# Optimization experiments

Measured on AMD Instinct MI355X. Metric: run time of the kernel, lower is better.

## Reference

```python
import jax, jax.numpy as jnp
import numpy as np

EMBED_DIM = 256; NUM_HEADS = 8; NUM_LEVELS = 4; NUM_POINTS = 4; FFN_DIM = 1024
SHAPES = [(128, 128), (64, 64), (32, 32), (16, 16)]
LN_EPS = 1e-5


def setup_inputs() -> dict:
    key = jax.random.key(0)
    ks = jax.random.split(key, 12)
    B = 2; C = EMBED_DIM
    Lin = sum(h * w for h, w in SHAPES)
    starts = np.concatenate([[0], np.cumsum([h * w for h, w in SHAPES])[:-1]])
    MLP2 = NUM_HEADS * NUM_LEVELS * NUM_POINTS
    p = lambda k, *s: jax.random.normal(k, s, jnp.float32) * 0.05
    return {
        "src": jax.random.normal(ks[0], (B, Lin, C), jnp.float32),
        "pos": jax.random.normal(ks[1], (B, Lin, C), jnp.float32),
        "reference_points": jax.random.uniform(ks[2], (B, Lin, NUM_LEVELS, 2), jnp.float32),
        "Wv": p(ks[3], C, C), "bv": jnp.zeros((C,), jnp.float32),
        "Wo": p(ks[4], C, MLP2 * 2),
        "bo": jax.random.uniform(ks[5], (MLP2 * 2,), jnp.float32, -2.0, 2.0),
        "Wa": p(ks[6], C, MLP2), "ba": jnp.zeros((MLP2,), jnp.float32),
        "Wout": p(ks[7], C, C), "bout": jnp.zeros((C,), jnp.float32),
        "gamma": jnp.ones((C,), jnp.float32), "beta": jnp.zeros((C,), jnp.float32),
        "W1": p(ks[8], C, FFN_DIM), "b1": jnp.zeros((FFN_DIM,), jnp.float32),
        "W2": p(ks[9], FFN_DIM, C), "b2": jnp.zeros((C,), jnp.float32),
        "spatial_shapes": jnp.array(SHAPES, dtype=jnp.int32),
        "level_start_index": jnp.array(starts, dtype=jnp.int32),
        "padding_mask": jnp.zeros((B, Lin), dtype=bool),
    }


def _layer_norm(x, g, b):
    m = jnp.mean(x, axis=-1, keepdims=True)
    v = jnp.mean((x - m) ** 2, axis=-1, keepdims=True)
    return (x - m) * jax.lax.rsqrt(v + LN_EPS) * g + b


def _bilinear_sample(val, loc, H, W):
    # val: [B, M, H*W, D]; loc: [B, M, Q, P, 2] normalized [0,1] (x, y)
    # matches torch grid_sample(align_corners=False, padding_mode='zeros')
    x = loc[..., 0] * W - 0.5
    y = loc[..., 1] * H - 0.5
    x0 = jnp.floor(x); y0 = jnp.floor(y)
    lx = x - x0; ly = y - y0
    x0 = x0.astype(jnp.int32); y0 = y0.astype(jnp.int32)
    Bm, M, Q, P = x0.shape
    out = jnp.zeros(val.shape[:2] + (Q, P, val.shape[-1]), val.dtype)
    corners = ((0, 0, (1 - lx) * (1 - ly)), (1, 0, lx * (1 - ly)),
               (0, 1, (1 - lx) * ly), (1, 1, lx * ly))
    for dx, dy, w in corners:
        xi = x0 + dx; yi = y0 + dy
        valid = (xi >= 0) & (xi < W) & (yi >= 0) & (yi < H)
        idx = jnp.clip(yi, 0, H - 1) * W + jnp.clip(xi, 0, W - 1)  # [B,M,Q,P]
        g = jnp.take_along_axis(val, idx.reshape(Bm, M, Q * P, 1), axis=2)
        g = g.reshape(Bm, M, Q, P, -1)
        out = out + (w * valid)[..., None] * g
    return out  # [B, M, Q, P, D]


def _forward(src, pos, reference_points, Wv, bv, Wo, bo, Wa, ba, Wout, bout,
             gamma, beta, W1, b1, W2, b2, spatial_shapes, level_start_index,
             padding_mask):
    M, L, P = NUM_HEADS, NUM_LEVELS, NUM_POINTS
    B, Lin, C = src.shape
    D = C // M
    shapes = np.asarray(spatial_shapes)          # static level geometry
    starts = np.asarray(level_start_index)
    query = src + pos
    value = src @ Wv + bv
    value = jnp.where(padding_mask[..., None], 0.0, value)
    value = value.reshape(B, Lin, M, D).transpose(0, 2, 1, 3)  # [B,M,Lin,D]
    Lq = query.shape[1]
    off = (query @ Wo + bo).reshape(B, Lq, M, L, P, 2)
    attn = jax.nn.softmax((query @ Wa + ba).reshape(B, Lq, M, L * P), axis=-1)
    attn = attn.reshape(B, Lq, M, L, P).transpose(0, 2, 1, 3, 4)  # [B,M,Lq,L,P]
    # offset normalizer is (W, H) per level
    normalizer = jnp.stack([spatial_shapes[:, 1], spatial_shapes[:, 0]], -1).astype(src.dtype)
    loc = reference_points[:, :, None, :, None, :] + off / normalizer[None, None, None, :, None, :]
    loc = loc.transpose(0, 2, 1, 3, 4, 5)  # [B,M,Lq,L,P,2]
    out = jnp.zeros((B, Lq, M, D), src.dtype)
    for l in range(L):
        H, W = int(shapes[l, 0]), int(shapes[l, 1])
        s = int(starts[l])
        vl = value[:, :, s:s + H * W, :]
        samp = _bilinear_sample(vl, loc[:, :, :, l], H, W)  # [B,M,Lq,P,D]
        out = out + jnp.einsum('bmqp,bmqpd->bqmd', attn[:, :, :, l], samp)
    src2 = out.reshape(B, Lq, C) @ Wout + bout
    x = _layer_norm(src + src2, gamma, beta)   # residual + norm (dropout is eval identity)
    h = jax.nn.relu(x @ W1 + b1)               # Mlp, no second residual in this module
    return h @ W2 + b2


def reference(src, pos, reference_points, Wv, bv, Wo, bo, Wa, ba, Wout, bout,
              gamma, beta, W1, b1, W2, b2, spatial_shapes, level_start_index,
              padding_mask):
    return _forward(src, pos, reference_points, Wv, bv, Wo, bo, Wa, ba, Wout,
                    bout, gamma, beta, W1, b1, W2, b2, spatial_shapes,
                    level_start_index, padding_mask)
```

## Files before the change

kernel.cpp:

```cpp
#include <hip/hip_runtime.h>
#include <hip/hip_bf16.h>
#include <math.h>

#define B_SZ   2
#define LIN    21760
#define C_DIM  256
#define M_H    8
#define D_H    32
#define NLEV   4
#define NPTS   4
#define FFN    1024
#define NTOK   (B_SZ * LIN)
#define LN_EPS 1e-5f

typedef __bf16 bf16;
typedef bf16  bf16x4 __attribute__((ext_vector_type(4)));
typedef bf16  bf16x8 __attribute__((ext_vector_type(8)));
typedef float f32x4  __attribute__((ext_vector_type(4)));

__device__ __constant__ int c_Ht[4] = {128, 64, 32, 16};
__device__ __constant__ int c_Wt[4] = {128, 64, 32, 16};
__device__ __constant__ int c_St[4] = {0, 16384, 20480, 21504};

static __device__ __forceinline__ float bf2f(unsigned short u) {
    union { float f; unsigned int i; } c;
    c.i = ((unsigned int)u) << 16;
    return c.f;
}

__global__ __launch_bounds__(256) void k_conv(const float* __restrict__ src,
                                              const float* __restrict__ pos,
                                              bf16* __restrict__ srcb,
                                              bf16* __restrict__ qb) {
    const int i = blockIdx.x * 256 + threadIdx.x;
    const float4 s4 = ((const float4*)src)[i];
    const float4 p4 = ((const float4*)pos)[i];
    bf16x4 sb, qb4;
    sb.x = (bf16)s4.x; sb.y = (bf16)s4.y; sb.z = (bf16)s4.z; sb.w = (bf16)s4.w;
    qb4.x = (bf16)(s4.x + p4.x); qb4.y = (bf16)(s4.y + p4.y);
    qb4.z = (bf16)(s4.z + p4.z); qb4.w = (bf16)(s4.w + p4.w);
    ((bf16x4*)srcb)[i] = sb;
    ((bf16x4*)qb)[i]   = qb4;
}

__global__ __launch_bounds__(256) void k_wt(const float* __restrict__ W,
                                            bf16* __restrict__ Wt,
                                            int K, int N, int nTilesN) {
    __shared__ float tile[32][33];
    const int bx = blockIdx.x % nTilesN;
    const int by = blockIdx.x / nTilesN;
    const int tx = threadIdx.x & 31, ty = threadIdx.x >> 5;
    const int n0 = bx * 32, k0 = by * 32;
#pragma unroll
    for (int i = 0; i < 32; i += 8)
        tile[ty + i][tx] = W[(long)(k0 + ty + i) * N + n0 + tx];
    __syncthreads();
#pragma unroll
    for (int i = 0; i < 32; i += 8)
        Wt[(long)(n0 + ty + i) * K + k0 + tx] = (bf16)tile[tx][ty + i];
}

#define GEMM_PROLOG(Aptr)                                                     \
    const int t = threadIdx.x;                                                \
    const int lane = t & 63, w = t >> 6;                                      \
    const int c0 = lane & 15, kg = lane >> 4;                                 \
    const long tok0 = (long)blockIdx.x * 32;                                  \
    {                                                                         \
        const bf16x8* src8 = (const bf16x8*)((Aptr) + tok0 * C_DIM);          \
        bf16x8* dst8 = (bf16x8*)xs;                                           \
        for (int i = t; i < 1024; i += 256)                                   \
            dst8[i ^ ((i >> 5) & 7)] = src8[i];                               \
    }                                                                         \
    __syncthreads();                                                          \
    bf16x8 afr[2][8];                                                         \
    _Pragma("unroll")                                                         \
    for (int mh = 0; mh < 2; ++mh) {                                          \
        const int m = mh * 16 + c0;                                           \
        _Pragma("unroll")                                                     \
        for (int kc = 0; kc < 8; ++kc) {                                      \
            const int chunk = m * 32 + kc * 4 + kg;                           \
            afr[mh][kc] = ((const bf16x8*)xs)[chunk ^ (m & 7)];               \
        }                                                                     \
    }

__global__ __launch_bounds__(256) void k_value_mfma(const bf16* __restrict__ A,
                                                    const bf16* __restrict__ Bw,
                                                    const float* __restrict__ bv,
                                                    bf16* __restrict__ value) {
    __shared__ bf16 xs[32 * 256];
    GEMM_PROLOG(A)

    const int b = (int)(tok0 / LIN);
    const int qbase = (int)(tok0 - (long)b * LIN);

#pragma unroll
    for (int nt = 0; nt < 4; ++nt) {
        const int n = w * 64 + nt * 16 + c0;
        f32x4 a0 = {0.f, 0.f, 0.f, 0.f};
        f32x4 a1 = {0.f, 0.f, 0.f, 0.f};
        const bf16* wrow = Bw + (long)n * 256 + kg * 8;
#pragma unroll
        for (int kc = 0; kc < 8; ++kc) {
            const bf16x8 bfr = *(const bf16x8*)(wrow + kc * 32);
            a0 = __builtin_amdgcn_mfma_f32_16x16x32_bf16(afr[0][kc], bfr, a0, 0, 0, 0);
            a1 = __builtin_amdgcn_mfma_f32_16x16x32_bf16(afr[1][kc], bfr, a1, 0, 0, 0);
        }
        const float bb = bv[n];
        const int m = n >> 5, d = n & 31;
        bf16* vb = value + ((long)(b * M_H + m) * LIN) * D_H + d;
#pragma unroll
        for (int r = 0; r < 4; ++r) {
            const int q0 = qbase + kg * 4 + r;
            vb[(long)q0 * D_H]        = (bf16)(a0[r] + bb);
            vb[(long)(q0 + 16) * D_H] = (bf16)(a1[r] + bb);
        }
    }
}

__global__ __launch_bounds__(256) void k_qloc_mfma(const bf16* __restrict__ A,
                                                   const bf16* __restrict__ Bw,
                                                   const float* __restrict__ bo,
                                                   const float* __restrict__ ba,
                                                   const float* __restrict__ refp,
                                                   float* __restrict__ loc,
                                                   float* __restrict__ att) {
    __shared__ bf16 xs[32 * 256];
    GEMM_PROLOG(A)

#pragma unroll
    for (int nt = 0; nt < 6; ++nt) {
        const int n = w * 96 + nt * 16 + c0;
        f32x4 a0 = {0.f, 0.f, 0.f, 0.f};
        f32x4 a1 = {0.f, 0.f, 0.f, 0.f};
        const bf16* wrow = Bw + (long)n * 256 + kg * 8;
#pragma unroll
        for (int kc = 0; kc < 8; ++kc) {
            const bf16x8 bfr = *(const bf16x8*)(wrow + kc * 32);
            a0 = __builtin_amdgcn_mfma_f32_16x16x32_bf16(afr[0][kc], bfr, a0, 0, 0, 0);
            a1 = __builtin_amdgcn_mfma_f32_16x16x32_bf16(afr[1][kc], bfr, a1, 0, 0, 0);
        }
        if (n < 256) {
            const int l = (n >> 3) & 3;
            const int c = n & 1;
            const float rnorm = 1.f / ((c == 0) ? (float)c_Wt[l] : (float)c_Ht[l]);
            const float bb = bo[n];
#pragma unroll
            for (int r = 0; r < 4; ++r) {
                const long t0 = tok0 + kg * 4 + r;
                const long t1 = t0 + 16;
                loc[t0 * C_DIM + n] = refp[t0 * 8 + l * 2 + c] + (a0[r] + bb) * rnorm;
                loc[t1 * C_DIM + n] = refp[t1 * 8 + l * 2 + c] + (a1[r] + bb) * rnorm;
            }
        } else {
            const int j = n - 256;
            const float bb = ba[j];
#pragma unroll
            for (int r = 0; r < 4; ++r) {
                const long t0 = tok0 + kg * 4 + r;
                att[t0 * 128 + j]        = a0[r] + bb;
                att[(t0 + 16) * 128 + j] = a1[r] + bb;
            }
        }
    }
}

__global__ __launch_bounds__(256) void k_samp(const unsigned short* __restrict__ value,
                                              const float* __restrict__ loc,
                                              const float* __restrict__ att,
                                              bf16* __restrict__ outb) {
    __shared__ int4   soff[128];
    __shared__ float4 swgt[128];
    const int t = threadIdx.x;
    const long tok = blockIdx.x;

    if (t < 128) {
        const float lg = att[tok * 128 + t];
        float mx = lg;
#pragma unroll
        for (int s = 1; s < 16; s <<= 1) mx = fmaxf(mx, __shfl_xor(mx, s));
        const float e = expf(lg - mx);
        float sm = e;
#pragma unroll
        for (int s = 1; s < 16; s <<= 1) sm += __shfl_xor(sm, s);
        const float a = e / sm;

        const float2 xy = ((const float2*)loc)[tok * 128 + t];
        const int l = (t >> 2) & 3;
        const int H = c_Ht[l], W = c_Wt[l], s0 = c_St[l];
        const float x = fmaf(xy.x, (float)W, -0.5f);
        const float y = fmaf(xy.y, (float)H, -0.5f);
        const float x0f = floorf(x), y0f = floorf(y);
        const float fx = x - x0f, fy = y - y0f;
        const int x0 = (int)x0f, y0 = (int)y0f;

        const int xi0 = min(max(x0, 0), W - 1);
        const int xi1 = min(max(x0 + 1, 0), W - 1);
        const int yi0 = min(max(y0, 0), H - 1);
        const int yi1 = min(max(y0 + 1, 0), H - 1);
        const float mx0 = (x0 >= 0 && x0 < W) ? 1.f : 0.f;
        const float mx1 = (x0 + 1 < W)        ? 1.f : 0.f;
        const float my0 = (y0 >= 0 && y0 < H) ? 1.f : 0.f;
        const float my1 = (y0 + 1 < H)        ? 1.f : 0.f;
        const float gx0 = (1.f - fx) * mx0, gx1 = fx * ((x0 + 1 >= 0) ? mx1 : 0.f);
        const float gy0 = (1.f - fy) * my0, gy1 = fy * ((y0 + 1 >= 0) ? my1 : 0.f);

        const int r0 = (s0 + yi0 * W) * D_H;
        const int r1 = (s0 + yi1 * W) * D_H;
        soff[t] = (int4){r0 + xi0 * D_H, r0 + xi1 * D_H, r1 + xi0 * D_H, r1 + xi1 * D_H};
        swgt[t] = (float4){a * gx0 * gy0, a * gx1 * gy0, a * gx0 * gy1, a * gx1 * gy1};
    }
    __syncthreads();

    const int m = t >> 5, d = t & 31;
    const int b = (int)(tok / LIN);
    const unsigned short* vb = value + ((long)(b * M_H + m)) * LIN * D_H + d;

    float acc = 0.f;
#pragma unroll
    for (int p = 0; p < 16; ++p) {
        const int jj = m * 16 + p;
        const int4   o = soff[jj];
        const float4 wv = swgt[jj];
        acc = fmaf(bf2f(vb[o.x]), wv.x, acc);
        acc = fmaf(bf2f(vb[o.y]), wv.y, acc);
        acc = fmaf(bf2f(vb[o.z]), wv.z, acc);
        acc = fmaf(bf2f(vb[o.w]), wv.w, acc);
    }
    outb[tok * C_DIM + t] = (bf16)acc;
}

__global__ __launch_bounds__(256) void k_post_mfma(const bf16* __restrict__ A,
                                                   const bf16* __restrict__ Bw,
                                                   const float* __restrict__ bout,
                                                   const float* __restrict__ src,
                                                   const float* __restrict__ g_,
                                                   const float* __restrict__ be_,
                                                   bf16* __restrict__ xb) {
    __shared__ bf16 xs[32 * 256];
    __shared__ float yt[32][256];
    GEMM_PROLOG(A)

#pragma unroll
    for (int nt = 0; nt < 4; ++nt) {
        const int n = w * 64 + nt * 16 + c0;
        f32x4 a0 = {0.f, 0.f, 0.f, 0.f};
        f32x4 a1 = {0.f, 0.f, 0.f, 0.f};
        const bf16* wrow = Bw + (long)n * 256 + kg * 8;
#pragma unroll
        for (int kc = 0; kc < 8; ++kc) {
            const bf16x8 bfr = *(const bf16x8*)(wrow + kc * 32);
            a0 = __builtin_amdgcn_mfma_f32_16x16x32_bf16(afr[0][kc], bfr, a0, 0, 0, 0);
            a1 = __builtin_amdgcn_mfma_f32_16x16x32_bf16(afr[1][kc], bfr, a1, 0, 0, 0);
        }
        const float bb = bout[n];
#pragma unroll
        for (int r = 0; r < 4; ++r) {
            const int row = kg * 4 + r;
            yt[row][n]      = a0[r] + bb + src[(tok0 + row) * C_DIM + n];
            yt[row + 16][n] = a1[r] + bb + src[(tok0 + row + 16) * C_DIM + n];
        }
    }
    __syncthreads();

    const float4 g4 = ((const float4*)g_)[lane];
    const float4 b4 = ((const float4*)be_)[lane];
#pragma unroll
    for (int rr = 0; rr < 8; ++rr) {
        const int row = w * 8 + rr;
        const float4 y4 = *(const float4*)&yt[row][lane * 4];
        float s1 = y4.x + y4.y + y4.z + y4.w;
        float s2 = y4.x * y4.x + y4.y * y4.y + y4.z * y4.z + y4.w * y4.w;
#pragma unroll
        for (int s = 1; s < 64; s <<= 1) {
            s1 += __shfl_xor(s1, s);
            s2 += __shfl_xor(s2, s);
        }
        const float mean = s1 * (1.f / 256.f);
        const float var  = s2 * (1.f / 256.f) - mean * mean;
        const float inv  = rsqrtf(var + LN_EPS);
        bf16x4 o;
        o.x = (bf16)((y4.x - mean) * inv * g4.x + b4.x);
        o.y = (bf16)((y4.y - mean) * inv * g4.y + b4.y);
        o.z = (bf16)((y4.z - mean) * inv * g4.z + b4.z);
        o.w = (bf16)((y4.w - mean) * inv * g4.w + b4.w);
        *(bf16x4*)(xb + (tok0 + row) * C_DIM + lane * 4) = o;
    }
}

__global__ __launch_bounds__(256) void k_ffn_mfma(const bf16* __restrict__ x,
                                                  const bf16* __restrict__ W1t,
                                                  const float* __restrict__ b1,
                                                  const bf16* __restrict__ W2t,
                                                  const float* __restrict__ b2,
                                                  float* __restrict__ out) {
    __shared__ bf16 xs[32 * 256];
    __shared__ bf16 hs[32 * 1024];
    const int t = threadIdx.x;
    const int lane = t & 63, w = t >> 6;
    const int c0 = lane & 15, kg = lane >> 4;
    const long tok0 = (long)blockIdx.x * 32;

    {
        const bf16x8* src8 = (const bf16x8*)(x + tok0 * C_DIM);
        bf16x8* dst8 = (bf16x8*)xs;
        for (int i = t; i < 32 * 32; i += 256)
            dst8[i ^ ((i >> 5) & 7)] = src8[i];
    }
    __syncthreads();

    bf16x8 afr[2][8];
#pragma unroll
    for (int mh = 0; mh < 2; ++mh) {
        const int m = mh * 16 + c0;
#pragma unroll
        for (int kc = 0; kc < 8; ++kc) {
            const int chunk = m * 32 + kc * 4 + kg;
            afr[mh][kc] = ((const bf16x8*)xs)[chunk ^ (m & 7)];
        }
    }

    for (int nt = 0; nt < 16; ++nt) {
        const int n = w * 256 + nt * 16 + c0;
        f32x4 acc0 = {0.f, 0.f, 0.f, 0.f};
        f32x4 acc1 = {0.f, 0.f, 0.f, 0.f};
        const bf16* wrow = W1t + (long)n * 256 + kg * 8;
#pragma unroll
        for (int kc = 0; kc < 8; ++kc) {
            const bf16x8 bfr = *(const bf16x8*)(wrow + kc * 32);
            acc0 = __builtin_amdgcn_mfma_f32_16x16x32_bf16(afr[0][kc], bfr, acc0, 0, 0, 0);
            acc1 = __builtin_amdgcn_mfma_f32_16x16x32_bf16(afr[1][kc], bfr, acc1, 0, 0, 0);
        }
        const float bb = b1[n];
#pragma unroll
        for (int r = 0; r < 4; ++r) {
            const int m0 = kg * 4 + r;
            const int m1 = m0 + 16;
            hs[(m0 * 1024 + n) ^ ((m0 & 7) << 3)] = (bf16)fmaxf(acc0[r] + bb, 0.f);
            hs[(m1 * 1024 + n) ^ ((m1 & 7) << 3)] = (bf16)fmaxf(acc1[r] + bb, 0.f);
        }
    }
    __syncthreads();

    f32x4 acc[2][4];
#pragma unroll
    for (int mh = 0; mh < 2; ++mh)
#pragma unroll
        for (int nt = 0; nt < 4; ++nt)
            acc[mh][nt] = (f32x4){0.f, 0.f, 0.f, 0.f};

    for (int kc = 0; kc < 32; ++kc) {
        const int kb = kc * 32 + kg * 8;
        const int mA = c0, mB = 16 + c0;
        const bf16x8 a0 = *(const bf16x8*)&hs[(mA * 1024 + kb) ^ ((mA & 7) << 3)];
        const bf16x8 a1 = *(const bf16x8*)&hs[(mB * 1024 + kb) ^ ((mB & 7) << 3)];
#pragma unroll
        for (int nt = 0; nt < 4; ++nt) {
            const int n = w * 64 + nt * 16 + c0;
            const bf16x8 bfr = *(const bf16x8*)&W2t[(long)n * FFN + kb];
            acc[0][nt] = __builtin_amdgcn_mfma_f32_16x16x32_bf16(a0, bfr, acc[0][nt], 0, 0, 0);
            acc[1][nt] = __builtin_amdgcn_mfma_f32_16x16x32_bf16(a1, bfr, acc[1][nt], 0, 0, 0);
        }
    }

#pragma unroll
    for (int nt = 0; nt < 4; ++nt) {
        const int n = w * 64 + nt * 16 + c0;
        const float bb = b2[n];
#pragma unroll
        for (int r = 0; r < 4; ++r) {
            out[(tok0 + kg * 4 + r) * C_DIM + n]      = acc[0][nt][r] + bb;
            out[(tok0 + 16 + kg * 4 + r) * C_DIM + n] = acc[1][nt][r] + bb;
        }
    }
}

extern "C" void kernel_launch(void* const* d_in, const int* in_sizes, int n_in,
                              void* d_out, int out_size, void* d_ws, size_t ws_size,
                              hipStream_t stream) {
    const float* src   = (const float*)d_in[0];
    const float* pos   = (const float*)d_in[1];
    const float* refp  = (const float*)d_in[2];
    const float* Wv    = (const float*)d_in[3];
    const float* bv    = (const float*)d_in[4];
    const float* Wo    = (const float*)d_in[5];
    const float* bo    = (const float*)d_in[6];
    const float* Wa    = (const float*)d_in[7];
    const float* ba    = (const float*)d_in[8];
    const float* Wout  = (const float*)d_in[9];
    const float* bout  = (const float*)d_in[10];
    const float* gamma = (const float*)d_in[11];
    const float* beta  = (const float*)d_in[12];
    const float* W1    = (const float*)d_in[13];
    const float* b1    = (const float*)d_in[14];
    const float* W2    = (const float*)d_in[15];
    const float* b2    = (const float*)d_in[16];

    const size_t N256 = (size_t)NTOK * C_DIM;
    bf16*  srcb = (bf16*)d_ws;
    bf16*  qb   = srcb + N256;
    bf16*  val  = qb + N256;
    float* loc  = (float*)(val + N256);
    float* att  = loc + N256;
    bf16*  Wvt  = (bf16*)(att + (size_t)NTOK * 128);
    bf16*  Wqt  = Wvt + 256 * 256;
    bf16*  Woutt= Wqt + 384 * 256;
    bf16*  W1t  = Woutt + 256 * 256;
    bf16*  W2t  = W1t + (size_t)FFN * C_DIM;
    bf16*  outb = srcb;
    bf16*  xb   = qb;

    dim3 blk(256);
    k_conv<<<NTOK * C_DIM / 4 / 256, blk, 0, stream>>>(src, pos, srcb, qb);
    k_wt<<<64,  blk, 0, stream>>>(Wv,   Wvt,           C_DIM, C_DIM, 8);
    k_wt<<<64,  blk, 0, stream>>>(Wo,   Wqt,           C_DIM, C_DIM, 8);
    k_wt<<<32,  blk, 0, stream>>>(Wa,   Wqt + 256*256, C_DIM, 128,   4);
    k_wt<<<64,  blk, 0, stream>>>(Wout, Woutt,         C_DIM, C_DIM, 8);
    k_wt<<<256, blk, 0, stream>>>(W1,   W1t,           C_DIM, FFN,   32);
    k_wt<<<256, blk, 0, stream>>>(W2,   W2t,           FFN,   C_DIM, 8);

    k_value_mfma<<<NTOK / 32, blk, 0, stream>>>(srcb, Wvt, bv, val);
    k_qloc_mfma <<<NTOK / 32, blk, 0, stream>>>(qb, Wqt, bo, ba, refp, loc, att);
    k_samp      <<<NTOK,      blk, 0, stream>>>((const unsigned short*)val, loc, att, outb);
    k_post_mfma <<<NTOK / 32, blk, 0, stream>>>(outb, Woutt, bout, src, gamma, beta, xb);
    k_ffn_mfma  <<<NTOK / 32, blk, 0, stream>>>(xb, W1t, b1, W2t, b2, (float*)d_out);
}
```

Measured before the change: 437.9 us.

## Split fused FFN kernel into two kernels staging hidden activations in global memory

The fused FFN kernel, which kept the 32x1024 hidden tile and the input tile in about 80KB of shared memory, is split into two kernels. The first computes relu(xW1+b1) and writes bf16 hidden activations to a workspace buffer that reuses the now-dead value/loc/att region. The second reads them back to compute the W2 projection. This removes the shared-memory footprint and the block barriers to raise occupancy, at the cost of an extra global-memory round trip for the large hidden tensor and one more launch.

```diff
diff --git a/kernel.cpp b/kernel.cpp
--- a/kernel.cpp
+++ b/kernel.cpp
@@ -287,59 +287,53 @@
     }
 }
 
-__global__ __launch_bounds__(256) void k_ffn_mfma(const bf16* __restrict__ x,
-                                                  const bf16* __restrict__ W1t,
-                                                  const float* __restrict__ b1,
-                                                  const bf16* __restrict__ W2t,
-                                                  const float* __restrict__ b2,
-                                                  float* __restrict__ out) {
-    __shared__ bf16 xs[32 * 256];
-    __shared__ bf16 hs[32 * 1024];
+__global__ __launch_bounds__(256) void k_ffn1(const bf16* __restrict__ x,
+                                              const bf16* __restrict__ W1t,
+                                              const float* __restrict__ b1,
+                                              bf16* __restrict__ h) {
     const int t = threadIdx.x;
     const int lane = t & 63, w = t >> 6;
     const int c0 = lane & 15, kg = lane >> 4;
     const long tok0 = (long)blockIdx.x * 32;
 
-    {
-        const bf16x8* src8 = (const bf16x8*)(x + tok0 * C_DIM);
-        bf16x8* dst8 = (bf16x8*)xs;
-        for (int i = t; i < 32 * 32; i += 256)
-            dst8[i ^ ((i >> 5) & 7)] = src8[i];
-    }
-    __syncthreads();
-
     bf16x8 afr[2][8];
 #pragma unroll
     for (int mh = 0; mh < 2; ++mh) {
-        const int m = mh * 16 + c0;
-#pragma unroll
-        for (int kc = 0; kc < 8; ++kc) {
-            const int chunk = m * 32 + kc * 4 + kg;
-            afr[mh][kc] = ((const bf16x8*)xs)[chunk ^ (m & 7)];
-        }
+        const long row = tok0 + mh * 16 + c0;
+#pragma unroll
+        for (int kc = 0; kc < 8; ++kc)
+            afr[mh][kc] = *(const bf16x8*)(x + row * C_DIM + kc * 32 + kg * 8);
     }
 
     for (int nt = 0; nt < 16; ++nt) {
         const int n = w * 256 + nt * 16 + c0;
-        f32x4 acc0 = {0.f, 0.f, 0.f, 0.f};
-        f32x4 acc1 = {0.f, 0.f, 0.f, 0.f};
+        f32x4 a0 = {0.f, 0.f, 0.f, 0.f};
+        f32x4 a1 = {0.f, 0.f, 0.f, 0.f};
         const bf16* wrow = W1t + (long)n * 256 + kg * 8;
 #pragma unroll
         for (int kc = 0; kc < 8; ++kc) {
             const bf16x8 bfr = *(const bf16x8*)(wrow + kc * 32);
-            acc0 = __builtin_amdgcn_mfma_f32_16x16x32_bf16(afr[0][kc], bfr, acc0, 0, 0, 0);
-            acc1 = __builtin_amdgcn_mfma_f32_16x16x32_bf16(afr[1][kc], bfr, acc1, 0, 0, 0);
+            a0 = __builtin_amdgcn_mfma_f32_16x16x32_bf16(afr[0][kc], bfr, a0, 0, 0, 0);
+            a1 = __builtin_amdgcn_mfma_f32_16x16x32_bf16(afr[1][kc], bfr, a1, 0, 0, 0);
         }
         const float bb = b1[n];
+        bf16* hp = h + (tok0 + kg * 4) * FFN + n;
 #pragma unroll
         for (int r = 0; r < 4; ++r) {
-            const int m0 = kg * 4 + r;
-            const int m1 = m0 + 16;
-            hs[(m0 * 1024 + n) ^ ((m0 & 7) << 3)] = (bf16)fmaxf(acc0[r] + bb, 0.f);
-            hs[(m1 * 1024 + n) ^ ((m1 & 7) << 3)] = (bf16)fmaxf(acc1[r] + bb, 0.f);
-        }
-    }
-    __syncthreads();
+            hp[(long)r * FFN]        = (bf16)fmaxf(a0[r] + bb, 0.f);
+            hp[(long)(r + 16) * FFN] = (bf16)fmaxf(a1[r] + bb, 0.f);
+        }
+    }
+}
+
+__global__ __launch_bounds__(256) void k_ffn2(const bf16* __restrict__ h,
+                                              const bf16* __restrict__ W2t,
+                                              const float* __restrict__ b2,
+                                              float* __restrict__ out) {
+    const int t = threadIdx.x;
+    const int lane = t & 63, w = t >> 6;
+    const int c0 = lane & 15, kg = lane >> 4;
+    const long tok0 = (long)blockIdx.x * 32;
 
     f32x4 acc[2][4];
 #pragma unroll
@@ -348,15 +342,16 @@
         for (int nt = 0; nt < 4; ++nt)
             acc[mh][nt] = (f32x4){0.f, 0.f, 0.f, 0.f};
 
+    const bf16* ha = h + (tok0 + c0) * FFN + kg * 8;
+    const bf16* hb = ha + 16 * FFN;
     for (int kc = 0; kc < 32; ++kc) {
-        const int kb = kc * 32 + kg * 8;
-        const int mA = c0, mB = 16 + c0;
-        const bf16x8 a0 = *(const bf16x8*)&hs[(mA * 1024 + kb) ^ ((mA & 7) << 3)];
-        const bf16x8 a1 = *(const bf16x8*)&hs[(mB * 1024 + kb) ^ ((mB & 7) << 3)];
+        const int kb = kc * 32;
+        const bf16x8 a0 = *(const bf16x8*)(ha + kb);
+        const bf16x8 a1 = *(const bf16x8*)(hb + kb);
 #pragma unroll
         for (int nt = 0; nt < 4; ++nt) {
             const int n = w * 64 + nt * 16 + c0;
-            const bf16x8 bfr = *(const bf16x8*)&W2t[(long)n * FFN + kb];
+            const bf16x8 bfr = *(const bf16x8*)(W2t + (long)n * FFN + kb + kg * 8);
             acc[0][nt] = __builtin_amdgcn_mfma_f32_16x16x32_bf16(a0, bfr, acc[0][nt], 0, 0, 0);
             acc[1][nt] = __builtin_amdgcn_mfma_f32_16x16x32_bf16(a1, bfr, acc[1][nt], 0, 0, 0);
         }
@@ -408,6 +403,7 @@
     bf16*  W2t  = W1t + (size_t)FFN * C_DIM;
     bf16*  outb = srcb;
     bf16*  xb   = qb;
+    bf16*  hbuf = val;
 
     dim3 blk(256);
     k_conv<<<NTOK * C_DIM / 4 / 256, blk, 0, stream>>>(src, pos, srcb, qb);
@@ -422,5 +418,6 @@
     k_qloc_mfma <<<NTOK / 32, blk, 0, stream>>>(qb, Wqt, bo, ba, refp, loc, att);
     k_samp      <<<NTOK,      blk, 0, stream>>>((const unsigned short*)val, loc, att, outb);
     k_post_mfma <<<NTOK / 32, blk, 0, stream>>>(outb, Woutt, bout, src, gamma, beta, xb);
-    k_ffn_mfma  <<<NTOK / 32, blk, 0, stream>>>(xb, W1t, b1, W2t, b2, (float*)d_out);
-}
+    k_ffn1      <<<NTOK / 32, blk, 0, stream>>>(xb, W1t, b1, hbuf);
+    k_ffn2      <<<NTOK / 32, blk, 0, stream>>>(hbuf, W2t, b2, (float*)d_out);
+}
```

Result: slower. 496.5 us (+13.4%).
